# Performance work log

Hardware: AMD Instinct MI355X
Metric: run time of the kernel (lower is better)

Reference implementation:

```python
import jax, jax.numpy as jnp
import numpy as np

DT = 0.01

def setup_inputs() -> dict:
    key = jax.random.key(0)
    k1, k2, k3, k4 = jax.random.split(key, 4)
    B, D_MODEL, D_LATENT = 32, 2048, 512
    z0 = jax.random.normal(k1, (B, D_LATENT), dtype=jnp.float32)
    h = jax.random.normal(k2, (B, D_MODEL), dtype=jnp.float32)
    # nn.Linear(d_latent, d_model-1): weight (d_model-1, d_latent), bias (d_model-1,)
    W_lie_w = jax.random.normal(k3, (D_MODEL - 1, D_LATENT), dtype=jnp.float32) * (1.0 / np.sqrt(D_LATENT))
    W_lie_b = jax.random.normal(k4, (D_MODEL - 1,), dtype=jnp.float32) * 0.01
    return {"z0": z0, "h": h, "W_lie_w": W_lie_w, "W_lie_b": W_lie_b}

def reference(z0, h, W_lie_w, W_lie_b):
    B, d = h.shape
    half_dt = DT / 2.0
    # Lie generator coefficients: v = tanh(W z0 + b), shape (B, d-1)
    v = jnp.tanh(jnp.einsum('bl,dl->bd', z0, W_lie_w) + W_lie_b)
    sub = half_dt * v    # subdiagonal of A = I - dt/2 * Omega
    sup = -half_dt * v   # superdiagonal
    # Dense (B, d, d) tridiagonal matrix (faithful to torch.diag_embed build)
    i = jnp.arange(d - 1)
    A = jnp.zeros((B, d, d), dtype=jnp.float32)
    A = A.at[:, jnp.arange(d), jnp.arange(d)].set(1.0)
    A = A.at[:, i + 1, i].set(sub)
    A = A.at[:, i, i + 1].set(sup)
    # RHS = (I + dt/2 * Omega) h
    super_contrib = half_dt * v * h[:, 1:]   # (B, d-1)
    sub_contrib = half_dt * v * h[:, :-1]    # (B, d-1)
    rhs = h + jnp.pad(super_contrib, ((0, 0), (0, 1))) - jnp.pad(sub_contrib, ((0, 0), (1, 0)))
    # Dense LU solve (same math as torch.linalg.lu_factor + lu_solve)
    x = jnp.linalg.solve(A, rhs[..., None])[..., 0]
    return x.astype(h.dtype)
```

## Files before the change

### kernel.cpp

```cpp
#include <hip/hip_runtime.h>
#include <hip/hip_bf16.h>

#define HALF_DT 0.005f

typedef __attribute__((ext_vector_type(8))) short short8;
typedef __attribute__((ext_vector_type(4))) float f32x4;

static __device__ inline short f2bf(float f) {
    __hip_bfloat16 b = __float2bfloat16(f);
    union { __hip_bfloat16 b; short s; } u; u.b = b;
    return u.s;
}

static __device__ inline short8 cvt8(const float* __restrict__ p) {
    float4 lo = *reinterpret_cast<const float4*>(p);
    float4 hi = *reinterpret_cast<const float4*>(p + 4);
    short8 r;
    r[0] = f2bf(lo.x); r[1] = f2bf(lo.y); r[2] = f2bf(lo.z); r[3] = f2bf(lo.w);
    r[4] = f2bf(hi.x); r[5] = f2bf(hi.y); r[6] = f2bf(hi.z); r[7] = f2bf(hi.w);
    return r;
}

__global__ __launch_bounds__(256) void v_mfma_kernel(
    const float* __restrict__ z0,
    const float* __restrict__ W,
    const float* __restrict__ bias,
    float* __restrict__ p_ws)
{
    __shared__ float part[2][64][4];

    const int tid   = threadIdx.x;
    const int wave  = tid >> 6;
    const int lane  = tid & 63;
    const int half  = wave & 1;
    const int khalf = wave >> 1;
    const int m     = lane & 15;
    const int q     = lane >> 4;
    const int col   = blockIdx.x * 16 + m;
    const int wcol  = (col < 2046) ? col : 2046;

    const float* zA = z0 + (half * 16 + m) * 512 + khalf * 256 + 8 * q;
    const float* wB = W + wcol * 512 + khalf * 256 + 8 * q;

    f32x4 acc = {0.f, 0.f, 0.f, 0.f};
    #pragma unroll 4
    for (int k0 = 0; k0 < 256; k0 += 32) {
        short8 a = cvt8(zA + k0);
        short8 b = cvt8(wB + k0);
        acc = __builtin_amdgcn_mfma_f32_16x16x32_bf16(a, b, acc, 0, 0, 0);
    }

    if (khalf == 1) {
        #pragma unroll
        for (int r = 0; r < 4; ++r) part[half][lane][r] = acc[r];
    }
    __syncthreads();
    if (khalf == 1) return;

    if (col < 2047) {
        const float bv = bias[col];
        #pragma unroll
        for (int r = 0; r < 4; ++r) {
            const int b = half * 16 + 4 * q + r;
            p_ws[b * 2048 + col] = HALF_DT * tanhf(acc[r] + part[half][lane][r] + bv);
        }
    }
}

__global__ __launch_bounds__(256) void solve2_kernel(
    const float* __restrict__ h,
    const float* __restrict__ p_ws,
    float* __restrict__ out)
{
    __shared__ float hl [520];
    __shared__ float p_l[520];
    __shared__ float u1l[520];

    const int b     = blockIdx.x >> 2;
    const int cbase = (blockIdx.x & 3) * 512;
    const int tid   = threadIdx.x;

    if (tid < 130) {
        const int i0 = cbase - 4 + 4 * tid;
        float4 hv = make_float4(0.f, 0.f, 0.f, 0.f);
        float4 pv = make_float4(0.f, 0.f, 0.f, 0.f);
        if (i0 >= 0 && i0 + 3 < 2048) {
            hv = *reinterpret_cast<const float4*>(h    + b * 2048 + i0);
            pv = *reinterpret_cast<const float4*>(p_ws + b * 2048 + i0);
            if (i0 + 3 == 2047) pv.w = 0.f;
        }
        *reinterpret_cast<float4*>(&hl [4 * tid]) = hv;
        *reinterpret_cast<float4*>(&p_l[4 * tid]) = pv;
    }
    __syncthreads();

    for (int c = 1 + tid; c <= 518; c += 256)
        u1l[c] = p_l[c - 1] * hl[c - 1] - p_l[c] * hl[c + 1];
    __syncthreads();

    #pragma unroll
    for (int k = 0; k < 2; ++k) {
        const int c = 4 + tid + k * 256;
        const float u2 = p_l[c - 1] * u1l[c - 1] - p_l[c] * u1l[c + 1];
        out[b * 2048 + cbase + (c - 4)] = hl[c] - 2.f * (u1l[c] - u2);
    }
}

extern "C" void kernel_launch(void* const* d_in, const int* in_sizes, int n_in,
                              void* d_out, int out_size, void* d_ws, size_t ws_size,
                              hipStream_t stream) {
    const float* z0   = (const float*)d_in[0];
    const float* h    = (const float*)d_in[1];
    const float* W    = (const float*)d_in[2];
    const float* bias = (const float*)d_in[3];
    float* out  = (float*)d_out;
    float* p_ws = (float*)d_ws;

    v_mfma_kernel<<<128, 256, 0, stream>>>(z0, W, bias, p_ws);
    solve2_kernel<<<128, 256, 0, stream>>>(h, p_ws, out);
}
```

Baseline: 12.50 us.

## Preload GEMM operands upfront, use fast tanh, and split solve over more blocks

The GEMM kernel now issues all of its z0 and W float4 loads into registers before the MFMA loop, so every load is in flight at once instead of being spread across unrolled iterations. tanhf is replaced by an exp-based fast_tanh, which is cheaper but less accurate near zero and overflows to inf for large inputs, where it still gives the right answer. The solve kernel's tile shrinks from 512 to 256 columns and it launches 256 blocks, giving each thread one output and more blocks across CUs. The cost is higher register pressure in the GEMM kernel and more halo reloads in the solve.

After: 12.24 us. 2.1% less time.

```diff
diff --git a/kernel.cpp b/kernel.cpp
--- a/kernel.cpp
+++ b/kernel.cpp
@@ -12,13 +12,15 @@
     return u.s;
 }
 
-static __device__ inline short8 cvt8(const float* __restrict__ p) {
-    float4 lo = *reinterpret_cast<const float4*>(p);
-    float4 hi = *reinterpret_cast<const float4*>(p + 4);
+static __device__ inline short8 cvt8v(float4 lo, float4 hi) {
     short8 r;
     r[0] = f2bf(lo.x); r[1] = f2bf(lo.y); r[2] = f2bf(lo.z); r[3] = f2bf(lo.w);
     r[4] = f2bf(hi.x); r[5] = f2bf(hi.y); r[6] = f2bf(hi.z); r[7] = f2bf(hi.w);
     return r;
+}
+
+static __device__ inline float fast_tanh(float x) {
+    return 1.f - 2.f / (__expf(2.f * x) + 1.f);
 }
 
 __global__ __launch_bounds__(256) void v_mfma_kernel(
@@ -39,14 +41,26 @@
     const int col   = blockIdx.x * 16 + m;
     const int wcol  = (col < 2046) ? col : 2046;
 
-    const float* zA = z0 + (half * 16 + m) * 512 + khalf * 256 + 8 * q;
-    const float* wB = W + wcol * 512 + khalf * 256 + 8 * q;
+    const float4* zA4 = reinterpret_cast<const float4*>(z0 + (half * 16 + m) * 512 + khalf * 256) + 2 * q;
+    const float4* wB4 = reinterpret_cast<const float4*>(W + wcol * 512 + khalf * 256) + 2 * q;
+
+    float4 wraw[16], zraw[16];
+    #pragma unroll
+    for (int s = 0; s < 8; ++s) {
+        wraw[2 * s]     = wB4[s * 8];
+        wraw[2 * s + 1] = wB4[s * 8 + 1];
+    }
+    #pragma unroll
+    for (int s = 0; s < 8; ++s) {
+        zraw[2 * s]     = zA4[s * 8];
+        zraw[2 * s + 1] = zA4[s * 8 + 1];
+    }
 
     f32x4 acc = {0.f, 0.f, 0.f, 0.f};
-    #pragma unroll 4
-    for (int k0 = 0; k0 < 256; k0 += 32) {
-        short8 a = cvt8(zA + k0);
-        short8 b = cvt8(wB + k0);
+    #pragma unroll
+    for (int s = 0; s < 8; ++s) {
+        short8 a = cvt8v(zraw[2 * s], zraw[2 * s + 1]);
+        short8 b = cvt8v(wraw[2 * s], wraw[2 * s + 1]);
         acc = __builtin_amdgcn_mfma_f32_16x16x32_bf16(a, b, acc, 0, 0, 0);
     }
 
@@ -62,7 +76,7 @@
         #pragma unroll
         for (int r = 0; r < 4; ++r) {
             const int b = half * 16 + 4 * q + r;
-            p_ws[b * 2048 + col] = HALF_DT * tanhf(acc[r] + part[half][lane][r] + bv);
+            p_ws[b * 2048 + col] = HALF_DT * fast_tanh(acc[r] + part[half][lane][r] + bv);
         }
     }
 }
@@ -72,15 +86,15 @@
     const float* __restrict__ p_ws,
     float* __restrict__ out)
 {
-    __shared__ float hl [520];
-    __shared__ float p_l[520];
-    __shared__ float u1l[520];
+    __shared__ float hl [264];
+    __shared__ float p_l[264];
+    __shared__ float u1l[264];
 
-    const int b     = blockIdx.x >> 2;
-    const int cbase = (blockIdx.x & 3) * 512;
+    const int b     = blockIdx.x >> 3;
+    const int cbase = (blockIdx.x & 7) * 256;
     const int tid   = threadIdx.x;
 
-    if (tid < 130) {
+    if (tid < 66) {
         const int i0 = cbase - 4 + 4 * tid;
         float4 hv = make_float4(0.f, 0.f, 0.f, 0.f);
         float4 pv = make_float4(0.f, 0.f, 0.f, 0.f);
@@ -94,13 +108,12 @@
     }
     __syncthreads();
 
-    for (int c = 1 + tid; c <= 518; c += 256)
+    for (int c = 1 + tid; c <= 262; c += 256)
         u1l[c] = p_l[c - 1] * hl[c - 1] - p_l[c] * hl[c + 1];
     __syncthreads();
 
-    #pragma unroll
-    for (int k = 0; k < 2; ++k) {
-        const int c = 4 + tid + k * 256;
+    {
+        const int c = 4 + tid;
         const float u2 = p_l[c - 1] * u1l[c - 1] - p_l[c] * u1l[c + 1];
         out[b * 2048 + cbase + (c - 4)] = hl[c] - 2.f * (u1l[c] - u2);
     }
@@ -117,5 +130,5 @@
     float* p_ws = (float*)d_ws;
 
     v_mfma_kernel<<<128, 256, 0, stream>>>(z0, W, bias, p_ws);
-    solve2_kernel<<<128, 256, 0, stream>>>(h, p_ws, out);
+    solve2_kernel<<<256, 256, 0, stream>>>(h, p_ws, out);
 }
```
